# Performance work log

Hardware: AMD Instinct MI355X
Metric: run time of the kernel (lower is better)

The kernel has to match this reference:

```python
import jax, jax.numpy as jnp
import numpy as np

N = 100000   # nodes
E = 1600000  # edges
H = 128      # num_features == hidden_size
C = 64       # num_classes
BN_EPS = 1e-5


def setup_inputs() -> dict:
    key = jax.random.key(0)
    ks = jax.random.split(key, 11)
    return {
        "x": jax.random.normal(ks[0], (N, H), jnp.float32),
        "edge_index": jax.random.randint(ks[1], (2, E), 0, N, dtype=jnp.int32),
        "edge_attr": jax.random.normal(ks[2], (E,), jnp.float32),
        "conv_w": jax.random.normal(ks[3], (2, 3, H, H), jnp.float32) / np.sqrt(H).astype(np.float32),
        "conv_b": jax.random.normal(ks[4], (2, 3, H), jnp.float32) * 0.1,
        "bn_g": jax.random.uniform(ks[5], (2, 3, H), jnp.float32, 0.5, 1.5),
        "bn_b": jax.random.normal(ks[6], (2, 3, H), jnp.float32) * 0.1,
        "bn_m": jax.random.normal(ks[7], (2, 3, H), jnp.float32) * 0.1,
        "bn_v": jax.random.uniform(ks[8], (2, 3, H), jnp.float32, 0.5, 1.5),
        "fc_w": jax.random.normal(ks[9], (H, C), jnp.float32) / np.sqrt(H).astype(np.float32),
        "fc_b": jax.random.normal(ks[10], (C,), jnp.float32) * 0.1,
    }


def _gin_conv(h, edge_index, w, b, g, beta, m, v):
    # GIN: out = MLP((1+eps)*x + sum_{j in N(i)} x_j), eps=0 (PyG default)
    src, dst = edge_index[0], edge_index[1]
    agg = jax.ops.segment_sum(h[src], dst, num_segments=N)  # [N,H] scatter-add
    h = h + agg
    for i in range(3):  # Linear -> BatchNorm1d (eval stats) -> ReLU
        h = h @ w[i] + b[i]
        h = (h - m[i]) * jax.lax.rsqrt(v[i] + BN_EPS) * g[i] + beta[i]
        h = jax.nn.relu(h)
    return h


def reference(x, edge_index, edge_attr, conv_w, conv_b, bn_g, bn_b, bn_m, bn_v, fc_w, fc_b):
    # edge_attr is ignored by default PyG GINConv (no edge weighting in GIN)
    h = jax.nn.relu(_gin_conv(x, edge_index, conv_w[0], conv_b[0], bn_g[0], bn_b[0], bn_m[0], bn_v[0]))
    h = jax.nn.relu(_gin_conv(h, edge_index, conv_w[1], conv_b[1], bn_g[1], bn_b[1], bn_m[1], bn_v[1]))
    # dropout is identity in eval mode
    logits = h @ fc_w + fc_b  # [N,C]
    return jax.nn.log_softmax(logits, axis=1)
```

## Files before the change

### kernel.cpp

```cpp
#include <hip/hip_runtime.h>

#define NN 100000
#define NE 1600000
#define HF 128
#define NC 64
#define AP 136
#define NB 391
#define BSH 8
#define BMASK 255
#define BCAP 4608

typedef __bf16 bf16x8 __attribute__((ext_vector_type(8)));
typedef float  f32x4  __attribute__((ext_vector_type(4)));
typedef unsigned short us8 __attribute__((ext_vector_type(8)));

__device__ __forceinline__ unsigned short f2b(float x) {
  unsigned int u = __float_as_uint(x);
  u += 0x7FFFu + ((u >> 16) & 1u);
  return (unsigned short)(u >> 16);
}
__device__ __forceinline__ float b2f(unsigned short b) {
  return __uint_as_float(((unsigned int)b) << 16);
}

__global__ __launch_bounds__(512) void prologue_bin(const float* __restrict__ x,
                                                    unsigned short* __restrict__ xb,
                                                    const float* __restrict__ conv_w,
                                                    const float* __restrict__ conv_b,
                                                    const float* __restrict__ bn_g,
                                                    const float* __restrict__ bn_b,
                                                    const float* __restrict__ bn_m,
                                                    const float* __restrict__ bn_v,
                                                    const float* __restrict__ fc_w,
                                                    unsigned short* __restrict__ wt,
                                                    unsigned short* __restrict__ wtf,
                                                    float* __restrict__ sarr,
                                                    float* __restrict__ tarr,
                                                    int* __restrict__ gcur,
                                                    const int* __restrict__ src,
                                                    const int* __restrict__ dst,
                                                    unsigned int* __restrict__ binned) {
  __shared__ int hist[NB];
  int t = threadIdx.x;
  int idx = blockIdx.x * 512 + t;
  {
    size_t i = (size_t)idx * 8;
    float4 a = *(const float4*)(x + i);
    float4 b = *(const float4*)(x + i + 4);
    us8 v = { f2b(a.x), f2b(a.y), f2b(a.z), f2b(a.w),
              f2b(b.x), f2b(b.y), f2b(b.z), f2b(b.w) };
    *(us8*)(xb + i) = v;
  }
  if (idx < 6 * HF * HF) {
    int j  = idx & 7;
    int m  = (idx >> 3) & 15;
    int q  = (idx >> 7) & 3;
    int nt = (idx >> 9) & 7;
    int k0 = (idx >> 12) & 3;
    int ls = idx >> 14;
    int k = k0 * 32 + q * 8 + j;
    int n = nt * 16 + m;
    wt[idx] = f2b(conv_w[(ls * HF + k) * HF + n]);
  }
  if (idx < HF * NC) {
    int j  = idx & 7;
    int m  = (idx >> 3) & 15;
    int q  = (idx >> 7) & 3;
    int nt = (idx >> 9) & 3;
    int k0 = idx >> 11;
    int k = k0 * 32 + q * 8 + j;
    int c = nt * 16 + m;
    wtf[idx] = f2b(fc_w[k * NC + c]);
  }
  if (idx < 6 * HF) {
    float s = bn_g[idx] * rsqrtf(bn_v[idx] + 1e-5f);
    sarr[idx] = s;
    tarr[idx] = (conv_b[idx] - bn_m[idx]) * s + bn_b[idx];
  }
  if (blockIdx.x < NB) {
    if (t < NB) hist[t] = 0;
    __syncthreads();
    int base = blockIdx.x * 4096;
    int sv[8], dv[8];
    #pragma unroll
    for (int j = 0; j < 8; j++) {
      int e = base + j * 512 + t;
      bool ok = e < NE;
      dv[j] = ok ? dst[e] : -1;
      sv[j] = ok ? src[e] : 0;
      if (ok) atomicAdd(&hist[dv[j] >> BSH], 1);
    }
    __syncthreads();
    if (t < NB) {
      int c = hist[t];
      if (c) hist[t] = t * BCAP + atomicAdd(&gcur[t], c);
    }
    __syncthreads();
    #pragma unroll
    for (int j = 0; j < 8; j++) {
      if (dv[j] >= 0) {
        int b = dv[j] >> BSH;
        int p = atomicAdd(&hist[b], 1);
        binned[p] = (unsigned int)sv[j] | ((unsigned int)(dv[j] & BMASK) << 17);
      }
    }
  }
}

__global__ __launch_bounds__(512) void build_csr(const unsigned int* __restrict__ binned,
                                                 const int* __restrict__ gcur,
                                                 int* __restrict__ offs,
                                                 int* __restrict__ deg,
                                                 int* __restrict__ csr) {
  __shared__ int ncnt[256];
  __shared__ int sm[256];
  int t = threadIdx.x;
  int b = blockIdx.x;
  int beg = b * BCAP;
  int cntb = gcur[b];
  if (t < 256) ncnt[t] = 0;
  __syncthreads();
  for (int e = beg + t; e < beg + cntb; e += 512) atomicAdd(&ncnt[binned[e] >> 17], 1);
  __syncthreads();
  int s = 0;
  if (t < 256) { s = ncnt[t]; sm[t] = s; }
  __syncthreads();
  for (int off = 1; off < 256; off <<= 1) {
    int u = (t < 256 && t >= off) ? sm[t - off] : 0;
    __syncthreads();
    if (t < 256) sm[t] += u;
    __syncthreads();
  }
  if (t < 256) {
    int ex = sm[t] - s + beg;
    int node = (b << BSH) + t;
    if (node < NN) { offs[node] = ex; deg[node] = s; }
    ncnt[t] = ex;
  }
  __syncthreads();
  for (int e = beg + t; e < beg + cntb; e += 512) {
    unsigned int u = binned[e];
    int p = atomicAdd(&ncnt[u >> 17], 1);
    csr[p] = (int)(u & 0x1FFFFu);
  }
}

__global__ __launch_bounds__(256) void aggregate(const unsigned short* __restrict__ h,
                                                 const int* __restrict__ offs,
                                                 const int* __restrict__ deg,
                                                 const int* __restrict__ csr,
                                                 unsigned short* __restrict__ out) {
  int wave = threadIdx.x >> 6;
  int lane = threadIdx.x & 63;
  int node = blockIdx.x * 4 + wave;
  if (node >= NN) return;
  int g  = lane >> 4;
  int sl = lane & 15;
  int beg = offs[node];
  int dg  = deg[node];

  float acc[8];
  if (g == 0) {
    us8 v = *(const us8*)(h + (size_t)node * HF + sl * 8);
    #pragma unroll
    for (int i = 0; i < 8; i++) acc[i] = b2f(v[i]);
  } else {
    #pragma unroll
    for (int i = 0; i < 8; i++) acc[i] = 0.f;
  }

  int e = beg + g;
  int last = beg + dg;
  for (; e + 4 < last; e += 8) {
    int s0 = csr[e];
    int s1 = csr[e + 4];
    us8 v0 = *(const us8*)(h + (size_t)s0 * HF + sl * 8);
    us8 v1 = *(const us8*)(h + (size_t)s1 * HF + sl * 8);
    #pragma unroll
    for (int i = 0; i < 8; i++) acc[i] += b2f(v0[i]);
    #pragma unroll
    for (int i = 0; i < 8; i++) acc[i] += b2f(v1[i]);
  }
  if (e < last) {
    int s0 = csr[e];
    us8 v0 = *(const us8*)(h + (size_t)s0 * HF + sl * 8);
    #pragma unroll
    for (int i = 0; i < 8; i++) acc[i] += b2f(v0[i]);
  }

  #pragma unroll
  for (int i = 0; i < 8; i++) {
    acc[i] += __shfl_xor(acc[i], 16, 64);
    acc[i] += __shfl_xor(acc[i], 32, 64);
  }
  if (g == 0) {
    us8 r;
    #pragma unroll
    for (int i = 0; i < 8; i++) r[i] = f2b(acc[i]);
    *(us8*)(out + (size_t)node * HF + sl * 8) = r;
  }
}

__device__ __forceinline__ void mlp3_body(const unsigned short* __restrict__ in,
                                          unsigned short* Ab,
                                          const unsigned short* __restrict__ wt,
                                          const float* __restrict__ sarr,
                                          const float* __restrict__ tarr,
                                          int layer, int row0, int wave, int lane,
                                          bf16x8 af[4]) {
  int m = lane & 15, q = lane >> 4;
  int node = row0 + wave * 16 + m;
  int nclamp = (node < NN) ? node : 0;
  #pragma unroll
  for (int k0 = 0; k0 < 4; k0++)
    af[k0] = *(const bf16x8*)(in + (size_t)nclamp * HF + k0 * 32 + q * 8);

  const unsigned short* wbase = wt + layer * 3 * 16384;
  #pragma unroll
  for (int sub = 0; sub < 3; sub++) {
    const unsigned short* wsub = wbase + sub * 16384;
    f32x4 acc[8];
    #pragma unroll
    for (int nt = 0; nt < 8; nt++) {
      acc[nt] = (f32x4){0.f, 0.f, 0.f, 0.f};
      #pragma unroll
      for (int k0 = 0; k0 < 4; k0++) {
        bf16x8 bf = *(const bf16x8*)(wsub + ((k0 * 8 + nt) * 64 + lane) * 8);
        acc[nt] = __builtin_amdgcn_mfma_f32_16x16x32_bf16(af[k0], bf, acc[nt], 0, 0, 0);
      }
    }
    const float* sp = sarr + (layer * 3 + sub) * HF;
    const float* tp = tarr + (layer * 3 + sub) * HF;
    #pragma unroll
    for (int nt = 0; nt < 8; nt++) {
      int c = nt * 16 + m;
      float sc = sp[c], sh = tp[c];
      #pragma unroll
      for (int i = 0; i < 4; i++) {
        int r = wave * 16 + q * 4 + i;
        float y = fmaxf(acc[nt][i] * sc + sh, 0.f);
        Ab[r * AP + c] = f2b(y);
      }
    }
    #pragma unroll
    for (int k0 = 0; k0 < 4; k0++)
      af[k0] = *(const bf16x8*)&Ab[(wave * 16 + m) * AP + k0 * 32 + q * 8];
  }
}

__global__ __launch_bounds__(256) void mlp3(const unsigned short* __restrict__ in,
                                            unsigned short* __restrict__ out,
                                            const unsigned short* __restrict__ wt,
                                            const float* __restrict__ sarr,
                                            const float* __restrict__ tarr) {
  __shared__ unsigned short Ab[64 * AP];
  int t = threadIdx.x;
  int lane = t & 63, wave = t >> 6;
  int row0 = blockIdx.x * 64;
  bf16x8 af[4];
  mlp3_body(in, Ab, wt, sarr, tarr, 0, row0, wave, lane, af);

  for (int it = 0; it < 4; it++) {
    int idx = it * 64 + lane;
    int r = wave * 16 + (idx >> 4);
    int c = (idx & 15) << 3;
    int gr = row0 + r;
    if (gr < NN) *(us8*)(out + (size_t)gr * HF + c) = *(const us8*)&Ab[r * AP + c];
  }
}

__global__ __launch_bounds__(256) void mlp3fc(const unsigned short* __restrict__ in,
                                              float* __restrict__ out,
                                              const unsigned short* __restrict__ wt,
                                              const float* __restrict__ sarr,
                                              const float* __restrict__ tarr,
                                              const unsigned short* __restrict__ wtf,
                                              const float* __restrict__ fc_b) {
  __shared__ unsigned short Ab[64 * AP];
  int t = threadIdx.x;
  int lane = t & 63, wave = t >> 6;
  int row0 = blockIdx.x * 64;
  int m = lane & 15, q = lane >> 4;
  bf16x8 af[4];
  mlp3_body(in, Ab, wt, sarr, tarr, 1, row0, wave, lane, af);

  f32x4 acc[4];
  #pragma unroll
  for (int nt = 0; nt < 4; nt++) {
    acc[nt] = (f32x4){0.f, 0.f, 0.f, 0.f};
    #pragma unroll
    for (int k0 = 0; k0 < 4; k0++) {
      bf16x8 bf = *(const bf16x8*)(wtf + ((k0 * 4 + nt) * 64 + lane) * 8);
      acc[nt] = __builtin_amdgcn_mfma_f32_16x16x32_bf16(af[k0], bf, acc[nt], 0, 0, 0);
    }
  }
  float v[4][4];
  #pragma unroll
  for (int nt = 0; nt < 4; nt++) {
    float b = fc_b[nt * 16 + m];
    #pragma unroll
    for (int i = 0; i < 4; i++) v[nt][i] = acc[nt][i] + b;
  }
  float mx[4], sum[4];
  #pragma unroll
  for (int i = 0; i < 4; i++) {
    mx[i] = fmaxf(fmaxf(v[0][i], v[1][i]), fmaxf(v[2][i], v[3][i]));
    mx[i] = fmaxf(mx[i], __shfl_xor(mx[i], 1, 64));
    mx[i] = fmaxf(mx[i], __shfl_xor(mx[i], 2, 64));
    mx[i] = fmaxf(mx[i], __shfl_xor(mx[i], 4, 64));
    mx[i] = fmaxf(mx[i], __shfl_xor(mx[i], 8, 64));
    sum[i] = __expf(v[0][i] - mx[i]) + __expf(v[1][i] - mx[i])
           + __expf(v[2][i] - mx[i]) + __expf(v[3][i] - mx[i]);
    sum[i] += __shfl_xor(sum[i], 1, 64);
    sum[i] += __shfl_xor(sum[i], 2, 64);
    sum[i] += __shfl_xor(sum[i], 4, 64);
    sum[i] += __shfl_xor(sum[i], 8, 64);
    sum[i] = __logf(sum[i]) + mx[i];
  }
  #pragma unroll
  for (int i = 0; i < 4; i++) {
    int gr = row0 + wave * 16 + q * 4 + i;
    if (gr < NN) {
      #pragma unroll
      for (int nt = 0; nt < 4; nt++)
        out[(size_t)gr * NC + nt * 16 + m] = v[nt][i] - sum[i];
    }
  }
}

extern "C" void kernel_launch(void* const* d_in, const int* in_sizes, int n_in,
                              void* d_out, int out_size, void* d_ws, size_t ws_size,
                              hipStream_t stream) {
  const float* x      = (const float*)d_in[0];
  const int*   ei     = (const int*)d_in[1];
  const float* conv_w = (const float*)d_in[3];
  const float* conv_b = (const float*)d_in[4];
  const float* bn_g   = (const float*)d_in[5];
  const float* bn_b   = (const float*)d_in[6];
  const float* bn_m   = (const float*)d_in[7];
  const float* bn_v   = (const float*)d_in[8];
  const float* fc_w   = (const float*)d_in[9];
  const float* fc_b   = (const float*)d_in[10];
  float* out = (float*)d_out;

  const int* srcI = ei;
  const int* dstI = ei + NE;

  unsigned short* Xb   = (unsigned short*)d_ws;
  unsigned short* Abuf = Xb + (size_t)NN * HF;
  unsigned short* Bbuf = Abuf + (size_t)NN * HF;
  int* gcur   = (int*)(Bbuf + (size_t)NN * HF);
  int* offs   = gcur + 512;
  int* deg    = offs + 100004;
  unsigned int* binned = (unsigned int*)(deg + 100004);
  int* csr    = (int*)(binned + (size_t)NB * BCAP);
  unsigned short* wt  = (unsigned short*)(csr + (size_t)NB * BCAP);
  unsigned short* wtf = wt + 6 * HF * HF;
  float* sarr = (float*)(wtf + HF * NC);
  float* tarr = sarr + 6 * HF;

  hipMemsetAsync(gcur, 0, sizeof(int) * NB, stream);
  prologue_bin<<<3125, 512, 0, stream>>>(x, Xb, conv_w, conv_b, bn_g, bn_b, bn_m, bn_v,
                                         fc_w, wt, wtf, sarr, tarr, gcur,
                                         srcI, dstI, binned);
  build_csr<<<NB, 512, 0, stream>>>(binned, gcur, offs, deg, csr);

  aggregate<<<NN / 4, 256, 0, stream>>>(Xb, offs, deg, csr, Abuf);
  mlp3<<<(NN + 63) / 64, 256, 0, stream>>>(Abuf, Bbuf, wt, sarr, tarr);
  aggregate<<<NN / 4, 256, 0, stream>>>(Bbuf, offs, deg, csr, Abuf);
  mlp3fc<<<(NN + 63) / 64, 256, 0, stream>>>(Abuf, out, wt, sarr, tarr, wtf, fc_b);
}
```

Baseline: 335.3 us.

## Preload neighbor indices per wave and unroll gathers with padded zero row

The aggregate kernel now has each lane load one neighbor index from the CSR, including the self node, into a register. Indices are then broadcast with shuffles so four row gathers can be in flight per group without dependent CSR loads in the loop. A zero padding row is added at index NN in each feature buffer so inactive slots read zeros instead of needing branches. Accumulation uses packed float2 adds with bit-shift bf16 unpacking. Nodes with degree of 64 or more fall back to a strided tail loop. The cost is a larger workspace layout and the added shuffles.

```diff
diff --git a/kernel.cpp b/kernel.cpp
--- a/kernel.cpp
+++ b/kernel.cpp
@@ -12,7 +12,9 @@
 
 typedef __bf16 bf16x8 __attribute__((ext_vector_type(8)));
 typedef float  f32x4  __attribute__((ext_vector_type(4)));
+typedef float  f32x2  __attribute__((ext_vector_type(2)));
 typedef unsigned short us8 __attribute__((ext_vector_type(8)));
+typedef unsigned int u32x4 __attribute__((ext_vector_type(4)));
 
 __device__ __forceinline__ unsigned short f2b(float x) {
   unsigned int u = __float_as_uint(x);
@@ -21,6 +23,16 @@
 }
 __device__ __forceinline__ float b2f(unsigned short b) {
   return __uint_as_float(((unsigned int)b) << 16);
+}
+
+__device__ __forceinline__ void addrow(f32x2 acc[4], u32x4 w) {
+  #pragma unroll
+  for (int i = 0; i < 4; i++) {
+    f32x2 p;
+    p.x = __uint_as_float(w[i] << 16);
+    p.y = __uint_as_float(w[i] & 0xFFFF0000u);
+    acc[i] += p;
+  }
 }
 
 __global__ __launch_bounds__(512) void prologue_bin(const float* __restrict__ x,
@@ -51,6 +63,10 @@
               f2b(b.x), f2b(b.y), f2b(b.z), f2b(b.w) };
     *(us8*)(xb + i) = v;
   }
+  if (idx < 3 * HF) {
+    int k = idx >> 7, jj = idx & 127;
+    xb[(size_t)k * (NN + 1) * HF + (size_t)NN * HF + jj] = 0;
+  }
   if (idx < 6 * HF * HF) {
     int j  = idx & 7;
     int m  = (idx >> 3) & 15;
@@ -153,50 +169,76 @@
   int wave = threadIdx.x >> 6;
   int lane = threadIdx.x & 63;
   int node = blockIdx.x * 4 + wave;
-  if (node >= NN) return;
   int g  = lane >> 4;
   int sl = lane & 15;
   int beg = offs[node];
   int dg  = deg[node];
-
-  float acc[8];
-  if (g == 0) {
-    us8 v = *(const us8*)(h + (size_t)node * HF + sl * 8);
-    #pragma unroll
-    for (int i = 0; i < 8; i++) acc[i] = b2f(v[i]);
-  } else {
-    #pragma unroll
-    for (int i = 0; i < 8; i++) acc[i] = 0.f;
-  }
-
-  int e = beg + g;
-  int last = beg + dg;
-  for (; e + 4 < last; e += 8) {
-    int s0 = csr[e];
-    int s1 = csr[e + 4];
-    us8 v0 = *(const us8*)(h + (size_t)s0 * HF + sl * 8);
-    us8 v1 = *(const us8*)(h + (size_t)s1 * HF + sl * 8);
-    #pragma unroll
-    for (int i = 0; i < 8; i++) acc[i] += b2f(v0[i]);
-    #pragma unroll
-    for (int i = 0; i < 8; i++) acc[i] += b2f(v1[i]);
-  }
-  if (e < last) {
-    int s0 = csr[e];
-    us8 v0 = *(const us8*)(h + (size_t)s0 * HF + sl * 8);
-    #pragma unroll
-    for (int i = 0; i < 8; i++) acc[i] += b2f(v0[i]);
-  }
-
-  #pragma unroll
-  for (int i = 0; i < 8; i++) {
-    acc[i] += __shfl_xor(acc[i], 16, 64);
-    acc[i] += __shfl_xor(acc[i], 32, 64);
+  int n  = dg + 1;
+  int nf = n < 64 ? n : 64;
+
+  int myidx = NN;
+  if (lane < nf) myidx = (lane == dg) ? node : csr[beg + lane];
+
+  f32x2 acc[4];
+  #pragma unroll
+  for (int i = 0; i < 4; i++) acc[i] = (f32x2){0.f, 0.f};
+
+  int K = (nf + 3) >> 2;
+  int j = 0;
+  for (; j + 3 < K; j += 4) {
+    int s0 = __shfl(myidx, (j + 0) * 4 + g);
+    int s1 = __shfl(myidx, (j + 1) * 4 + g);
+    int s2 = __shfl(myidx, (j + 2) * 4 + g);
+    int s3 = __shfl(myidx, (j + 3) * 4 + g);
+    u32x4 v0 = *(const u32x4*)(h + (size_t)s0 * HF + sl * 8);
+    u32x4 v1 = *(const u32x4*)(h + (size_t)s1 * HF + sl * 8);
+    u32x4 v2 = *(const u32x4*)(h + (size_t)s2 * HF + sl * 8);
+    u32x4 v3 = *(const u32x4*)(h + (size_t)s3 * HF + sl * 8);
+    addrow(acc, v0);
+    addrow(acc, v1);
+    addrow(acc, v2);
+    addrow(acc, v3);
+  }
+  for (; j + 1 < K; j += 2) {
+    int s0 = __shfl(myidx, (j + 0) * 4 + g);
+    int s1 = __shfl(myidx, (j + 1) * 4 + g);
+    u32x4 v0 = *(const u32x4*)(h + (size_t)s0 * HF + sl * 8);
+    u32x4 v1 = *(const u32x4*)(h + (size_t)s1 * HF + sl * 8);
+    addrow(acc, v0);
+    addrow(acc, v1);
+  }
+  if (j < K) {
+    int s0 = __shfl(myidx, j * 4 + g);
+    u32x4 v0 = *(const u32x4*)(h + (size_t)s0 * HF + sl * 8);
+    addrow(acc, v0);
+  }
+
+  if (dg >= 64) {
+    for (int e = beg + 64 + g; e < beg + dg; e += 4) {
+      int s = csr[e];
+      u32x4 v = *(const u32x4*)(h + (size_t)s * HF + sl * 8);
+      addrow(acc, v);
+    }
+    if (g == 0) {
+      u32x4 v = *(const u32x4*)(h + (size_t)node * HF + sl * 8);
+      addrow(acc, v);
+    }
+  }
+
+  #pragma unroll
+  for (int i = 0; i < 4; i++) {
+    acc[i].x += __shfl_xor(acc[i].x, 16, 64);
+    acc[i].y += __shfl_xor(acc[i].y, 16, 64);
+    acc[i].x += __shfl_xor(acc[i].x, 32, 64);
+    acc[i].y += __shfl_xor(acc[i].y, 32, 64);
   }
   if (g == 0) {
     us8 r;
     #pragma unroll
-    for (int i = 0; i < 8; i++) r[i] = f2b(acc[i]);
+    for (int i = 0; i < 4; i++) {
+      r[2 * i]     = f2b(acc[i].x);
+      r[2 * i + 1] = f2b(acc[i].y);
+    }
     *(us8*)(out + (size_t)node * HF + sl * 8) = r;
   }
 }
@@ -347,9 +389,9 @@
   const int* dstI = ei + NE;
 
   unsigned short* Xb   = (unsigned short*)d_ws;
-  unsigned short* Abuf = Xb + (size_t)NN * HF;
-  unsigned short* Bbuf = Abuf + (size_t)NN * HF;
-  int* gcur   = (int*)(Bbuf + (size_t)NN * HF);
+  unsigned short* Abuf = Xb + (size_t)(NN + 1) * HF;
+  unsigned short* Bbuf = Abuf + (size_t)(NN + 1) * HF;
+  int* gcur   = (int*)(Bbuf + (size_t)(NN + 1) * HF);
   int* offs   = gcur + 512;
   int* deg    = offs + 100004;
   unsigned int* binned = (unsigned int*)(deg + 100004);
```

New measurement: 327.7 us. 1.02x faster.
